# Kernel optimization log

Measured on AMD Instinct MI355X. Metric: run time of the kernel, lower is better.

## Reference

```python
import jax, jax.numpy as jnp
import numpy as np

B, S, H = 8, 512, 1024
NH = 8
DH = H // NH            # 128
INTER = 3072            # DebertaConfig default intermediate_size
SPAN = 512              # max_relative_positions (= max_position_embeddings)
LSTM_H = H // 2         # 512
EPS = 1e-7              # DeBERTa layer_norm_eps


def _ln(x, g, b):
    m = jnp.mean(x, -1, keepdims=True)
    v = jnp.var(x, -1, keepdims=True)
    return (x - m) / jnp.sqrt(v + EPS) * g + b


def _lstm_dir(x, Wih, Whh, bih, bhh, reverse):
    # x: [B,S,D]; precompute input projection for all steps
    xW = jnp.einsum('bsd,gd->sbg', x, Wih) + bih + bhh      # [S,B,4*Hd]
    Hd = Whh.shape[1]

    def step(carry, gx):
        h, c = carry
        gates = gx + h @ Whh.T
        i, f, g, o = jnp.split(gates, 4, axis=-1)           # torch gate order i,f,g,o
        i = jax.nn.sigmoid(i); f = jax.nn.sigmoid(f); o = jax.nn.sigmoid(o)
        g = jnp.tanh(g)
        c = f * c + i * g
        h = o * jnp.tanh(c)
        return (h, c), h

    h0 = jnp.zeros((x.shape[0], Hd), x.dtype)
    _, hs = jax.lax.scan(step, (h0, h0), xW, reverse=reverse)
    return jnp.swapaxes(hs, 0, 1)                            # [B,S,Hd]


def setup_inputs() -> dict:
    key = jax.random.key(0)
    ks = iter(jax.random.split(key, 40))

    def rn(shape, s=0.02):
        return jax.random.normal(next(ks), shape, jnp.float32) * s

    return {
        'x': jax.random.normal(next(ks), (B, S, H), jnp.float32),
        'pos_emb': rn((SPAN, H)),
        'emb_ln_g': jnp.ones((H,), jnp.float32),
        'emb_ln_b': jnp.zeros((H,), jnp.float32),
        'in_proj_w': rn((3 * H, H)),
        'q_bias': jnp.zeros((H,), jnp.float32),
        'v_bias': jnp.zeros((H,), jnp.float32),
        'rel_emb': rn((2 * SPAN, H)),
        'pos_proj_w': rn((H, H)),
        'pos_q_proj_w': rn((H, H)),
        'pos_q_proj_b': jnp.zeros((H,), jnp.float32),
        'attn_out_w': rn((H, H)),
        'attn_out_b': jnp.zeros((H,), jnp.float32),
        'attn_ln_g': jnp.ones((H,), jnp.float32),
        'attn_ln_b': jnp.zeros((H,), jnp.float32),
        'inter_w': rn((INTER, H)),
        'inter_b': jnp.zeros((INTER,), jnp.float32),
        'ffn_out_w': rn((H, INTER)),
        'ffn_out_b': jnp.zeros((H,), jnp.float32),
        'ffn_ln_g': jnp.ones((H,), jnp.float32),
        'ffn_ln_b': jnp.zeros((H,), jnp.float32),
        'Wih_f': rn((4 * LSTM_H, H)),
        'Whh_f': rn((4 * LSTM_H, LSTM_H)),
        'bih_f': jnp.zeros((4 * LSTM_H,), jnp.float32),
        'bhh_f': jnp.zeros((4 * LSTM_H,), jnp.float32),
        'Wih_r': rn((4 * LSTM_H, H)),
        'Whh_r': rn((4 * LSTM_H, LSTM_H)),
        'bih_r': jnp.zeros((4 * LSTM_H,), jnp.float32),
        'bhh_r': jnp.zeros((4 * LSTM_H,), jnp.float32),
    }


def reference(x, pos_emb, emb_ln_g, emb_ln_b, in_proj_w, q_bias, v_bias, rel_emb,
              pos_proj_w, pos_q_proj_w, pos_q_proj_b, attn_out_w, attn_out_b,
              attn_ln_g, attn_ln_b, inter_w, inter_b, ffn_out_w, ffn_out_b,
              ffn_ln_g, ffn_ln_b, Wih_f, Whh_f, bih_f, bhh_f, Wih_r, Whh_r,
              bih_r, bhh_r):
    # ---- DeBERTa embeddings: inputs_embeds + absolute positions, LayerNorm ----
    h = _ln(x + pos_emb[None, :S], emb_ln_g, emb_ln_b)

    # ---- disentangled self-attention (c2p + p2c) ----
    qkv = h @ in_proj_w.T                                    # [B,S,3H]
    q, k, v = jnp.split(qkv, 3, -1)
    q = q + q_bias
    v = v + v_bias

    def heads(t):
        return t.reshape(B, S, NH, DH).transpose(0, 2, 1, 3)  # [B,NH,S,DH]
    q, k, v = heads(q), heads(k), heads(v)

    scale_factor = 3.0                                       # 1 + len(['c2p','p2c'])
    q = q / jnp.sqrt(jnp.float32(DH) * scale_factor)
    scores = jnp.einsum('bhqd,bhkd->bhqk', q, k)             # [B,NH,S,S]

    rel_pos = jnp.arange(S)[:, None] - jnp.arange(S)[None, :]  # [S,S]

    # content -> position
    c2p_idx = jnp.clip(rel_pos + SPAN, 0, 2 * SPAN - 1)
    pos_key = (rel_emb @ pos_proj_w.T).reshape(2 * SPAN, NH, DH)
    c2p = jnp.einsum('bhqd,rhd->bhqr', q, pos_key)           # [B,NH,S,2*SPAN]
    c2p = jnp.take_along_axis(c2p, jnp.broadcast_to(c2p_idx[None, None], (B, NH, S, S)), axis=-1)

    # position -> content
    pos_q = (rel_emb @ pos_q_proj_w.T + pos_q_proj_b).reshape(2 * SPAN, NH, DH)
    pos_q = pos_q / jnp.sqrt(jnp.float32(DH) * scale_factor)
    p2c_idx = jnp.clip(-rel_pos + SPAN, 0, 2 * SPAN - 1)
    p2c = jnp.einsum('bhkd,rhd->bhkr', k, pos_q)             # [B,NH,S,2*SPAN]
    p2c = jnp.take_along_axis(p2c, jnp.broadcast_to(p2c_idx[None, None], (B, NH, S, S)), axis=-1)
    p2c = jnp.swapaxes(p2c, -1, -2)

    probs = jax.nn.softmax(scores + c2p + p2c, -1)
    ctx = jnp.einsum('bhqk,bhkd->bhqd', probs, v).transpose(0, 2, 1, 3).reshape(B, S, H)

    h = _ln(ctx @ attn_out_w.T + attn_out_b + h, attn_ln_g, attn_ln_b)
    inter = jax.nn.gelu(h @ inter_w.T + inter_b, approximate=False)
    h = _ln(inter @ ffn_out_w.T + ffn_out_b + h, ffn_ln_g, ffn_ln_b)

    # ---- bidirectional single-layer LSTM ----
    hf = _lstm_dir(h, Wih_f, Whh_f, bih_f, bhh_f, False)
    hr = _lstm_dir(h, Wih_r, Whh_r, bih_r, bhh_r, True)
    return jnp.concatenate([hf, hr], -1)                     # [B,S,H]
```

## Files before the change

kernel.cpp:

```cpp
#include <hip/hip_runtime.h>
#include <cstdint>


typedef __bf16 bf8_t __attribute__((ext_vector_type(8)));
typedef float f32x4 __attribute__((ext_vector_type(4)));
typedef unsigned int u32x4 __attribute__((ext_vector_type(4)));

__device__ __forceinline__ unsigned short f2bf(float f) {
  union { float f; unsigned int u; } v; v.f = f;
  unsigned int r = v.u + 0x7fffu + ((v.u >> 16) & 1u);
  return (unsigned short)(r >> 16);
}
__device__ __forceinline__ float bf2f(unsigned short s) {
  union { unsigned int u; float f; } v; v.u = ((unsigned int)s) << 16;
  return v.f;
}
__device__ __forceinline__ float bflo(unsigned int u) {
  union { unsigned int u; float f; } v; v.u = u << 16; return v.f;
}
__device__ __forceinline__ float bfhi(unsigned int u) {
  union { unsigned int u; float f; } v; v.u = u & 0xffff0000u; return v.f;
}

__device__ __forceinline__ void async16(const void* g, void* l) {
  __builtin_amdgcn_global_load_lds(
      (const __attribute__((address_space(1))) void*)g,
      (__attribute__((address_space(3))) void*)l, 16, 0, 0);
}

__device__ __forceinline__ void ld2_ic(const unsigned short* p0,
                                       const unsigned short* p1,
                                       u32x4& r0, u32x4& r1) {
  asm volatile("global_load_dwordx4 %0, %2, off sc0 sc1\n\t"
               "global_load_dwordx4 %1, %3, off sc0 sc1\n\t"
               "s_waitcnt vmcnt(0)"
               : "=v"(r0), "=v"(r1)
               : "v"(p0), "v"(p1)
               : "memory");
}
__device__ __forceinline__ void st_ic(unsigned short* p, u32x4 v) {
  asm volatile("global_store_dwordx4 %0, %1, off sc0 sc1"
               :: "v"(p), "v"(v) : "memory");
}
__device__ __forceinline__ int ld_flag_ic(const int* p) {
  int r;
  asm volatile("global_load_dword %0, %1, off sc0 sc1\n\t"
               "s_waitcnt vmcnt(0)"
               : "=v"(r) : "v"(p) : "memory");
  return r;
}
__device__ __forceinline__ void wait_vm0() {
  asm volatile("s_waitcnt vmcnt(0)" ::: "memory");
}

__global__ void k_sentinel(float* out) { out[0] = 1e30f; }

__global__ void k_cast_bf16(const float* __restrict__ in, unsigned short* __restrict__ out) {
  long i = ((long)blockIdx.x * 256 + threadIdx.x) * 4;
  float4 v = *(const float4*)(in + i);
  unsigned int a = (unsigned int)f2bf(v.x) | ((unsigned int)f2bf(v.y) << 16);
  unsigned int b = (unsigned int)f2bf(v.z) | ((unsigned int)f2bf(v.w) << 16);
  *(uint2*)(out + i) = make_uint2(a, b);
}

__global__ void k_build_bias(const float* qb, const float* vb, float* qkvBias,
                             const float* bihf, const float* bhhf, float* bsf,
                             const float* bihr, const float* bhhr, float* bsr) {
  int i = blockIdx.x * 256 + threadIdx.x;
  if (i < 3072) {
    float v;
    if (i < 1024) v = qb[i];
    else if (i < 2048) v = 0.f;
    else v = vb[i - 2048];
    qkvBias[i] = v;
  }
  if (i < 2048) {
    bsf[i] = bihf[i] + bhhf[i];
    bsr[i] = bihr[i] + bhhr[i];
  }
}

__global__ __launch_bounds__(256) void k_layernorm(
    const float* __restrict__ in, const float* __restrict__ res, unsigned int resMask,
    const float* __restrict__ gamma, const float* __restrict__ beta,
    float* __restrict__ outF, unsigned short* __restrict__ outB) {
  const int row = blockIdx.x;
  const int tid = threadIdx.x;
  float4 v = ((const float4*)(in + (long)row * 1024))[tid];
  if (res) {
    float4 r = ((const float4*)(res + (long)(row & resMask) * 1024))[tid];
    v.x += r.x; v.y += r.y; v.z += r.z; v.w += r.w;
  }
  float s = v.x + v.y + v.z + v.w;
  float q = v.x * v.x + v.y * v.y + v.z * v.z + v.w * v.w;
#pragma unroll
  for (int o = 32; o; o >>= 1) { s += __shfl_down(s, o); q += __shfl_down(q, o); }
  __shared__ float rs[4], rq[4];
  const int wave = tid >> 6, lane = tid & 63;
  if (lane == 0) { rs[wave] = s; rq[wave] = q; }
  __syncthreads();
  s = rs[0] + rs[1] + rs[2] + rs[3];
  q = rq[0] + rq[1] + rq[2] + rq[3];
  const float mean = s * (1.f / 1024.f);
  const float var = q * (1.f / 1024.f) - mean * mean;
  const float rstd = rsqrtf(var + 1e-7f);
  float4 g4 = ((const float4*)gamma)[tid];
  float4 b4 = ((const float4*)beta)[tid];
  float4 o4;
  o4.x = (v.x - mean) * rstd * g4.x + b4.x;
  o4.y = (v.y - mean) * rstd * g4.y + b4.y;
  o4.z = (v.z - mean) * rstd * g4.z + b4.z;
  o4.w = (v.w - mean) * rstd * g4.w + b4.w;
  if (outF) ((float4*)(outF + (long)row * 1024))[tid] = o4;
  if (outB) {
    unsigned int a = (unsigned int)f2bf(o4.x) | ((unsigned int)f2bf(o4.y) << 16);
    unsigned int b = (unsigned int)f2bf(o4.z) | ((unsigned int)f2bf(o4.w) << 16);
    ((uint2*)(outB + (long)row * 1024))[tid] = make_uint2(a, b);
  }
}

template <int MODE>
__global__ __launch_bounds__(256) void k_gemm_bt(
    const unsigned short* __restrict__ A, int lda,
    const unsigned short* __restrict__ Bm, int ldb,
    void* __restrict__ Cv, int ldc,
    int K, const float* __restrict__ bias, float scale) {
  __shared__ __align__(16) unsigned short As[128 * 32];
  __shared__ __align__(16) unsigned short Bs[128 * 32];
  const int tid = threadIdx.x;
  const int lane = tid & 63;
  const int wave = tid >> 6;
  const int n0 = blockIdx.x * 128;
  const int m0 = blockIdx.y * 128;
  const int srow = tid >> 2;
  const int scol = (tid & 3) * 8;
  const unsigned short* ag0 = A + (long)(m0 + srow) * lda + scol;
  const unsigned short* ag1 = A + (long)(m0 + 64 + srow) * lda + scol;
  const unsigned short* bg0 = Bm + (long)(n0 + srow) * ldb + scol;
  const unsigned short* bg1 = Bm + (long)(n0 + 64 + srow) * ldb + scol;
  unsigned short* asd0 = &As[(wave * 16) * 32];
  unsigned short* asd1 = &As[(64 + wave * 16) * 32];
  unsigned short* bsd0 = &Bs[(wave * 16) * 32];
  unsigned short* bsd1 = &Bs[(64 + wave * 16) * 32];
  const int wm = wave >> 1, wn = wave & 1;
  const int mrow = lane & 15;
  const int kq = (lane >> 4) * 8;
  const f32x4 vzero = {0.f, 0.f, 0.f, 0.f};
  f32x4 acc[4][4];
#pragma unroll
  for (int i = 0; i < 4; ++i)
#pragma unroll
    for (int j = 0; j < 4; ++j) acc[i][j] = vzero;

  const int nk = K >> 5;
  for (int kt = 0; kt < nk; ++kt) {
    if (kt) __syncthreads();
    async16(ag0, asd0); async16(ag1, asd1);
    async16(bg0, bsd0); async16(bg1, bsd1);
    ag0 += 32; ag1 += 32; bg0 += 32; bg1 += 32;
    __syncthreads();
    bf8_t af[4], bf[4];
#pragma unroll
    for (int i = 0; i < 4; ++i)
      af[i] = *(const bf8_t*)&As[(wm * 64 + i * 16 + mrow) * 32 + kq];
#pragma unroll
    for (int j = 0; j < 4; ++j)
      bf[j] = *(const bf8_t*)&Bs[(wn * 64 + j * 16 + mrow) * 32 + kq];
#pragma unroll
    for (int i = 0; i < 4; ++i)
#pragma unroll
      for (int j = 0; j < 4; ++j)
        acc[i][j] = __builtin_amdgcn_mfma_f32_16x16x32_bf16(af[i], bf[j], acc[i][j], 0, 0, 0);
  }
  const int quad = lane >> 4;
  const int cn = lane & 15;
  float* Cf = (float*)Cv;
  unsigned short* Cb = (unsigned short*)Cv;
#pragma unroll
  for (int i = 0; i < 4; ++i) {
#pragma unroll
    for (int j = 0; j < 4; ++j) {
#pragma unroll
      for (int r = 0; r < 4; ++r) {
        int row = m0 + wm * 64 + i * 16 + quad * 4 + r;
        int col = n0 + wn * 64 + j * 16 + cn;
        float v = acc[i][j][r];
        if (bias) v += bias[col];
        v *= scale;
        if (MODE == 2) v = 0.5f * v * (1.0f + erff(v * 0.70710678118654752f));
        long idx = (long)row * ldc + col;
        if (MODE == 0) Cf[idx] = v;
        else Cb[idx] = f2bf(v);
      }
    }
  }
}

__global__ __launch_bounds__(256) void k_attention(
    const unsigned short* __restrict__ qkv,
    const unsigned short* __restrict__ c2p,
    const unsigned short* __restrict__ p2c,
    unsigned short* __restrict__ ctx, int h) {
  const int tid = threadIdx.x;
  const int qt = blockIdx.x;
  const int b = blockIdx.y;
  const int q0 = qt * 16;
  __shared__ __align__(16) float sc[16][520];
  __shared__ __align__(16) float qs[16][128];

  for (int i = tid; i < 16 * 128; i += 256) {
    int ql = i >> 7, d = i & 127;
    qs[ql][d] = bf2f(qkv[((long)(b * 512 + q0 + ql)) * 3072 + h * 128 + d]);
  }
  __syncthreads();

  const float scale = 0.051031036307982884f;
  for (int pass = 0; pass < 2; ++pass) {
    const int k = tid + pass * 256;
    float4 kvf[32];
    const unsigned short* kp = qkv + ((long)(b * 512 + k)) * 3072 + 1024 + h * 128;
#pragma unroll
    for (int c = 0; c < 16; ++c) {
      uint4 u = ((const uint4*)kp)[c];
      kvf[2 * c + 0] = make_float4(bflo(u.x), bfhi(u.x), bflo(u.y), bfhi(u.y));
      kvf[2 * c + 1] = make_float4(bflo(u.z), bfhi(u.z), bflo(u.w), bfhi(u.w));
    }
    const unsigned short* pp = p2c + ((long)(b * 512 + k)) * 1024 + (q0 - k + 512);
    for (int ql = 0; ql < 16; ++ql) {
      float dot = 0.f;
#pragma unroll
      for (int dd = 0; dd < 32; ++dd) {
        float4 qf = ((const float4*)&qs[ql][0])[dd];
        dot += qf.x * kvf[dd].x + qf.y * kvf[dd].y + qf.z * kvf[dd].z + qf.w * kvf[dd].w;
      }
      sc[ql][k] = dot * scale + bf2f(pp[ql]);
    }
  }
  __syncthreads();

  const int wave = tid >> 6, lane = tid & 63;
#pragma unroll
  for (int rr = 0; rr < 4; ++rr) {
    const int r = wave * 4 + rr;
    const int q = q0 + r;
    const unsigned short* cp = c2p + ((long)(b * 512 + q)) * 1024 + (q + 512);
    float v[8];
#pragma unroll
    for (int i = 0; i < 8; ++i) {
      int k = lane + 64 * i;
      v[i] = sc[r][k] + bf2f(cp[-k]);
    }
    float m = v[0];
#pragma unroll
    for (int i = 1; i < 8; ++i) m = fmaxf(m, v[i]);
#pragma unroll
    for (int o = 32; o; o >>= 1) m = fmaxf(m, __shfl_xor(m, o));
    float ssum = 0.f;
#pragma unroll
    for (int i = 0; i < 8; ++i) { v[i] = __expf(v[i] - m); ssum += v[i]; }
#pragma unroll
    for (int o = 32; o; o >>= 1) ssum += __shfl_xor(ssum, o);
    const float inv = 1.0f / ssum;
#pragma unroll
    for (int i = 0; i < 8; ++i) sc[r][lane + 64 * i] = v[i] * inv;
  }
  __syncthreads();

  const int d = tid & 127;
  const int qg = tid >> 7;
  float acc[8] = {0, 0, 0, 0, 0, 0, 0, 0};
  const unsigned short* vp = qkv + ((long)(b * 512)) * 3072 + 2048 + h * 128 + d;
  for (int k = 0; k < 512; k += 4) {
    float v0 = bf2f(vp[(long)(k + 0) * 3072]);
    float v1 = bf2f(vp[(long)(k + 1) * 3072]);
    float v2 = bf2f(vp[(long)(k + 2) * 3072]);
    float v3 = bf2f(vp[(long)(k + 3) * 3072]);
#pragma unroll
    for (int qq = 0; qq < 8; ++qq) {
      float4 p = *(const float4*)&sc[qg * 8 + qq][k];
      acc[qq] += p.x * v0 + p.y * v1 + p.z * v2 + p.w * v3;
    }
  }
#pragma unroll
  for (int qq = 0; qq < 8; ++qq) {
    int q = q0 + qg * 8 + qq;
    ctx[((long)(b * 512 + q)) * 1024 + h * 128 + d] = f2bf(acc[qq]);
  }
}

__global__ __launch_bounds__(256) void k_lstm(
    const float* __restrict__ WhhF, const float* __restrict__ WhhR,
    const unsigned short* __restrict__ xWF, const unsigned short* __restrict__ xWR,
    float* __restrict__ out, unsigned short* __restrict__ hx,
    int* __restrict__ flags) {
  const int tid = threadIdx.x;
  const int lane = tid & 63;
  const int g = tid >> 6;
  const int dir = blockIdx.y;
  const int j0 = blockIdx.x * 16;
  const float* Whh = dir ? WhhR : WhhF;
  const unsigned short* xW = dir ? xWR : xWF;
  int* flg = flags + dir * 512;
  unsigned short* hxd = hx + (long)dir * 512 * 8 * 512;

  __shared__ __align__(16) unsigned short hT[16][520];
  __shared__ float gl[4][16][8];
  __shared__ __align__(16) unsigned short hs[8][16];

  const int m = lane & 15, quad = lane >> 4;
  bf8_t afr[16];
  {
    const float* wr = Whh + ((long)(g * 512 + j0 + m)) * 512 + quad * 8;
#pragma unroll
    for (int kt = 0; kt < 16; ++kt) {
      float4 f0 = *(const float4*)(wr + kt * 32);
      float4 f1 = *(const float4*)(wr + kt * 32 + 4);
      bf8_t a;
      a[0] = (__bf16)f0.x; a[1] = (__bf16)f0.y; a[2] = (__bf16)f0.z; a[3] = (__bf16)f0.w;
      a[4] = (__bf16)f1.x; a[5] = (__bf16)f1.y; a[6] = (__bf16)f1.z; a[7] = (__bf16)f1.w;
      afr[kt] = a;
    }
  }
  for (int i = tid; i < 16 * 520; i += 256) (&hT[0][0])[i] = 0;
  float cstate = 0.f;
  __syncthreads();

  for (int se = 0; se < 512; ++se) {
    const int s = dir ? 511 - se : se;
    uint2 uxw = make_uint2(0u, 0u);
    if (m < 8)
      uxw = *(const uint2*)(xW + ((long)(m * 512 + s)) * 2048 + g * 512 + j0 + quad * 4);

    if (se) {
      const int sp = dir ? s + 1 : s - 1;
      if (tid == 0) {
        while (ld_flag_ic(flg + (se - 1)) < 32) __builtin_amdgcn_s_sleep(1);
      }
      __syncthreads();
      const unsigned short* hxs = hxd + (long)sp * 4096;
      const int bb = tid >> 6;
      const int jc = (tid & 63) * 8;
      u32x4 r0, r1;
      ld2_ic(hxs + bb * 512 + jc, hxs + (bb + 4) * 512 + jc, r0, r1);
      *(u32x4*)&hT[bb][jc] = r0;
      *(u32x4*)&hT[bb + 4][jc] = r1;
      __syncthreads();
    }

    f32x4 acc0 = {0.f, 0.f, 0.f, 0.f}, acc1 = {0.f, 0.f, 0.f, 0.f};
#pragma unroll
    for (int t = 0; t < 8; ++t) {
      bf8_t b0 = *(const bf8_t*)&hT[m][(2 * t) * 32 + quad * 8];
      bf8_t b1 = *(const bf8_t*)&hT[m][(2 * t + 1) * 32 + quad * 8];
      acc0 = __builtin_amdgcn_mfma_f32_16x16x32_bf16(afr[2 * t], b0, acc0, 0, 0, 0);
      acc1 = __builtin_amdgcn_mfma_f32_16x16x32_bf16(afr[2 * t + 1], b1, acc1, 0, 0, 0);
    }
    if (m < 8) {
      gl[g][quad * 4 + 0][m] = acc0[0] + acc1[0] + bflo(uxw.x);
      gl[g][quad * 4 + 1][m] = acc0[1] + acc1[1] + bfhi(uxw.x);
      gl[g][quad * 4 + 2][m] = acc0[2] + acc1[2] + bflo(uxw.y);
      gl[g][quad * 4 + 3][m] = acc0[3] + acc1[3] + bfhi(uxw.y);
    }
    __syncthreads();
    if (tid < 128) {
      const int jj = tid >> 3, bb = tid & 7;
      float iv = gl[0][jj][bb], fv = gl[1][jj][bb];
      float gv = gl[2][jj][bb], ov = gl[3][jj][bb];
      float is = 1.f / (1.f + __expf(-iv));
      float fs = 1.f / (1.f + __expf(-fv));
      float gt = tanhf(gv);
      float os = 1.f / (1.f + __expf(-ov));
      cstate = fs * cstate + is * gt;
      float hv = os * tanhf(cstate);
      out[((long)(bb * 512 + s)) * 1024 + dir * 512 + j0 + jj] = hv;
      hs[bb][jj] = f2bf(hv);
    }
    __syncthreads();
    if (tid < 16) {
      const int b = tid >> 1, half = tid & 1;
      st_ic(hxd + (long)s * 4096 + b * 512 + j0 + half * 8,
            *(const u32x4*)&hs[b][half * 8]);
    }
    wait_vm0();
    __syncthreads();
    if (tid == 0)
      __hip_atomic_fetch_add(flg + se, 1, __ATOMIC_RELAXED, __HIP_MEMORY_SCOPE_AGENT);
  }
}

extern "C" void kernel_launch(void* const* d_in, const int* in_sizes, int n_in,
                              void* d_out, int out_size, void* d_ws, size_t ws_size,
                              hipStream_t stream) {
  const float* x         = (const float*)d_in[0];
  const float* pos_emb   = (const float*)d_in[1];
  const float* emb_ln_g  = (const float*)d_in[2];
  const float* emb_ln_b  = (const float*)d_in[3];
  const float* in_proj_w = (const float*)d_in[4];
  const float* q_bias    = (const float*)d_in[5];
  const float* v_bias    = (const float*)d_in[6];
  const float* rel_emb   = (const float*)d_in[7];
  const float* pos_proj_w   = (const float*)d_in[8];
  const float* pos_q_proj_w = (const float*)d_in[9];
  const float* pos_q_proj_b = (const float*)d_in[10];
  const float* attn_out_w = (const float*)d_in[11];
  const float* attn_out_b = (const float*)d_in[12];
  const float* attn_ln_g  = (const float*)d_in[13];
  const float* attn_ln_b  = (const float*)d_in[14];
  const float* inter_w    = (const float*)d_in[15];
  const float* inter_b    = (const float*)d_in[16];
  const float* ffn_out_w  = (const float*)d_in[17];
  const float* ffn_out_b  = (const float*)d_in[18];
  const float* ffn_ln_g   = (const float*)d_in[19];
  const float* ffn_ln_b   = (const float*)d_in[20];
  const float* Wih_f = (const float*)d_in[21];
  const float* Whh_f = (const float*)d_in[22];
  const float* bih_f = (const float*)d_in[23];
  const float* bhh_f = (const float*)d_in[24];
  const float* Wih_r = (const float*)d_in[25];
  const float* Whh_r = (const float*)d_in[26];
  const float* bih_r = (const float*)d_in[27];
  const float* bhh_r = (const float*)d_in[28];
  float* out = (float*)d_out;

  const size_t MB = 1ull << 20;
  const size_t NEED = 85 * MB;
  if (ws_size < NEED) {
    k_sentinel<<<dim3(1), dim3(1), 0, stream>>>(out);
    return;
  }
  char* ws = (char*)d_ws;
  typedef unsigned short u16;
  u16*   qkv_b    = (u16*)(ws + 0);
  float* attn_tmp = (float*)(ws + 0);
  u16*   xW_f     = (u16*)(ws + 0);
  u16*   h1_b     = (u16*)(ws + 16 * MB);
  u16*   xW_r     = (u16*)(ws + 16 * MB);
  float* h0_f     = (float*)(ws + 24 * MB);
  u16*   inter_bf = (u16*)(ws + 24 * MB);
  u16*   hx       = (u16*)(ws + 32 * MB);
  u16*   c2p_h    = (u16*)(ws + 40 * MB);
  u16*   p2c_h    = (u16*)(ws + 48 * MB);
  float* h1_f     = (float*)(ws + 48 * MB);
  u16*   h0_b     = (u16*)(ws + 64 * MB);
  u16*   ctx_b    = (u16*)(ws + 64 * MB);
  u16*   h2_b     = (u16*)(ws + 64 * MB);
  u16*   wscr     = (u16*)(ws + 72 * MB);
  u16*   relemb_b = (u16*)(ws + 78 * MB);
  u16*   poskey_b = (u16*)(ws + 80 * MB);
  u16*   posq_b   = (u16*)(ws + 82 * MB);
  float* bias_qkv = (float*)(ws + 84 * MB);
  float* bsum_f   = (float*)(ws + 84 * MB + 16 * 1024);
  float* bsum_r   = (float*)(ws + 84 * MB + 32 * 1024);
  int*   flags    = (int*)(ws + 84 * MB + 48 * 1024);
  float* ffn_tmp  = out;

  const float SCALE = 0.051031036307982884f;

  hipMemsetAsync(flags, 0, 1024 * 4, stream);

  auto cast = [&](const float* src, u16* dst, long n) {
    k_cast_bf16<<<dim3((unsigned)(n / 1024)), dim3(256), 0, stream>>>(src, dst);
  };

  k_build_bias<<<dim3(12), dim3(256), 0, stream>>>(q_bias, v_bias, bias_qkv,
                                                   bih_f, bhh_f, bsum_f,
                                                   bih_r, bhh_r, bsum_r);

  k_layernorm<<<dim3(4096), dim3(256), 0, stream>>>(x, pos_emb, 511u, emb_ln_g,
                                                    emb_ln_b, h0_f, h0_b);

  cast(in_proj_w, wscr, 3145728L);
  k_gemm_bt<1><<<dim3(24, 32), dim3(256), 0, stream>>>(
      h0_b, 1024, wscr, 1024, qkv_b, 3072, 1024, bias_qkv, 1.0f);

  cast(rel_emb, relemb_b, 1048576L);
  cast(pos_proj_w, wscr, 1048576L);
  k_gemm_bt<1><<<dim3(8, 8), dim3(256), 0, stream>>>(
      relemb_b, 1024, wscr, 1024, poskey_b, 1024, 1024, (const float*)nullptr, 1.0f);
  cast(pos_q_proj_w, wscr, 1048576L);
  k_gemm_bt<1><<<dim3(8, 8), dim3(256), 0, stream>>>(
      relemb_b, 1024, wscr, 1024, posq_b, 1024, 1024, pos_q_proj_b, SCALE);

  for (int h = 0; h < 8; ++h) {
    k_gemm_bt<1><<<dim3(8, 32), dim3(256), 0, stream>>>(
        qkv_b + h * 128, 3072, poskey_b + h * 128, 1024, c2p_h, 1024, 128,
        (const float*)nullptr, SCALE);
    k_gemm_bt<1><<<dim3(8, 32), dim3(256), 0, stream>>>(
        qkv_b + 1024 + h * 128, 3072, posq_b + h * 128, 1024, p2c_h, 1024, 128,
        (const float*)nullptr, 1.0f);
    k_attention<<<dim3(32, 8), dim3(256), 0, stream>>>(qkv_b, c2p_h, p2c_h, ctx_b, h);
  }

  cast(attn_out_w, wscr, 1048576L);
  k_gemm_bt<0><<<dim3(8, 32), dim3(256), 0, stream>>>(
      ctx_b, 1024, wscr, 1024, attn_tmp, 1024, 1024, attn_out_b, 1.0f);
  k_layernorm<<<dim3(4096), dim3(256), 0, stream>>>(attn_tmp, h0_f, 0xFFFFFFFFu,
                                                    attn_ln_g, attn_ln_b, h1_f, h1_b);

  cast(inter_w, wscr, 3145728L);
  k_gemm_bt<2><<<dim3(24, 32), dim3(256), 0, stream>>>(
      h1_b, 1024, wscr, 1024, inter_bf, 3072, 1024, inter_b, 1.0f);
  cast(ffn_out_w, wscr, 3145728L);
  k_gemm_bt<0><<<dim3(8, 32), dim3(256), 0, stream>>>(
      inter_bf, 3072, wscr, 3072, ffn_tmp, 1024, 3072, ffn_out_b, 1.0f);
  k_layernorm<<<dim3(4096), dim3(256), 0, stream>>>(ffn_tmp, h1_f, 0xFFFFFFFFu,
                                                    ffn_ln_g, ffn_ln_b,
                                                    (float*)nullptr, h2_b);

  cast(Wih_f, wscr, 2097152L);
  k_gemm_bt<1><<<dim3(16, 32), dim3(256), 0, stream>>>(
      h2_b, 1024, wscr, 1024, xW_f, 2048, 1024, bsum_f, 1.0f);
  cast(Wih_r, wscr, 2097152L);
  k_gemm_bt<1><<<dim3(16, 32), dim3(256), 0, stream>>>(
      h2_b, 1024, wscr, 1024, xW_r, 2048, 1024, bsum_r, 1.0f);

  k_lstm<<<dim3(32, 2), dim3(256), 0, stream>>>(Whh_f, Whh_r, xW_f, xW_r, out, hx, flags);

  (void)in_sizes; (void)n_in; (void)out_size;
}
```

Baseline: 2.440 ms.

## Replace LSTM flag counter sync with data-embedded nonzero sentinel polling

Removes the per-step atomic flag counter and its store-wait-barrier-atomic chain in the persistent LSTM kernel. Consumers now poll the hidden-state buffer directly, which is zeroed beforehand, until every bf16 value is nonzero, relying on forcing the low mantissa bit of each stored h to 1. The change also splits the MFMA accumulation into four independent chains and replaces tanhf with an exp-based formula. It adds a memset of the 8MB hx buffer and perturbs h by one bf16 ulp, and it assumes the 16-byte stores become visible atomically.

```diff
diff --git a/kernel.cpp b/kernel.cpp
--- a/kernel.cpp
+++ b/kernel.cpp
@@ -41,16 +41,6 @@
 __device__ __forceinline__ void st_ic(unsigned short* p, u32x4 v) {
   asm volatile("global_store_dwordx4 %0, %1, off sc0 sc1"
                :: "v"(p), "v"(v) : "memory");
-}
-__device__ __forceinline__ int ld_flag_ic(const int* p) {
-  int r;
-  asm volatile("global_load_dword %0, %1, off sc0 sc1\n\t"
-               "s_waitcnt vmcnt(0)"
-               : "=v"(r) : "v"(p) : "memory");
-  return r;
-}
-__device__ __forceinline__ void wait_vm0() {
-  asm volatile("s_waitcnt vmcnt(0)" ::: "memory");
 }
 
 __global__ void k_sentinel(float* out) { out[0] = 1e30f; }
@@ -291,8 +281,7 @@
 __global__ __launch_bounds__(256) void k_lstm(
     const float* __restrict__ WhhF, const float* __restrict__ WhhR,
     const unsigned short* __restrict__ xWF, const unsigned short* __restrict__ xWR,
-    float* __restrict__ out, unsigned short* __restrict__ hx,
-    int* __restrict__ flags) {
+    float* __restrict__ out, unsigned short* __restrict__ hx) {
   const int tid = threadIdx.x;
   const int lane = tid & 63;
   const int g = tid >> 6;
@@ -300,8 +289,7 @@
   const int j0 = blockIdx.x * 16;
   const float* Whh = dir ? WhhR : WhhF;
   const unsigned short* xW = dir ? xWR : xWF;
-  int* flg = flags + dir * 512;
-  unsigned short* hxd = hx + (long)dir * 512 * 8 * 512;
+  unsigned short* hxd = hx + (long)dir * 512 * 4096;
 
   __shared__ __align__(16) unsigned short hT[16][520];
   __shared__ float gl[4][16][8];
@@ -333,33 +321,42 @@
 
     if (se) {
       const int sp = dir ? s + 1 : s - 1;
-      if (tid == 0) {
-        while (ld_flag_ic(flg + (se - 1)) < 32) __builtin_amdgcn_s_sleep(1);
+      const unsigned short* hxs = hxd + (long)sp * 4096;
+      const unsigned short* p0 = hxs + (2 * g) * 512 + lane * 8;
+      const unsigned short* p1 = hxs + (2 * g + 1) * 512 + lane * 8;
+      u32x4 r0, r1;
+      for (;;) {
+        ld2_ic(p0, p1, r0, r1);
+        bool ok = true;
+#pragma unroll
+        for (int t = 0; t < 4; ++t) {
+          ok = ok && (r0[t] & 0xffffu) && (r0[t] >> 16) &&
+               (r1[t] & 0xffffu) && (r1[t] >> 16);
+        }
+        if (__ballot(ok) == 0xFFFFFFFFFFFFFFFFull) break;
       }
+      *(u32x4*)&hT[2 * g][lane * 8] = r0;
+      *(u32x4*)&hT[2 * g + 1][lane * 8] = r1;
       __syncthreads();
-      const unsigned short* hxs = hxd + (long)sp * 4096;
-      const int bb = tid >> 6;
-      const int jc = (tid & 63) * 8;
-      u32x4 r0, r1;
-      ld2_ic(hxs + bb * 512 + jc, hxs + (bb + 4) * 512 + jc, r0, r1);
-      *(u32x4*)&hT[bb][jc] = r0;
-      *(u32x4*)&hT[bb + 4][jc] = r1;
-      __syncthreads();
-    }
-
-    f32x4 acc0 = {0.f, 0.f, 0.f, 0.f}, acc1 = {0.f, 0.f, 0.f, 0.f};
-#pragma unroll
-    for (int t = 0; t < 8; ++t) {
-      bf8_t b0 = *(const bf8_t*)&hT[m][(2 * t) * 32 + quad * 8];
-      bf8_t b1 = *(const bf8_t*)&hT[m][(2 * t + 1) * 32 + quad * 8];
-      acc0 = __builtin_amdgcn_mfma_f32_16x16x32_bf16(afr[2 * t], b0, acc0, 0, 0, 0);
-      acc1 = __builtin_amdgcn_mfma_f32_16x16x32_bf16(afr[2 * t + 1], b1, acc1, 0, 0, 0);
+    }
+
+    f32x4 a0 = {0.f, 0.f, 0.f, 0.f}, a1 = a0, a2 = a0, a3 = a0;
+#pragma unroll
+    for (int t = 0; t < 4; ++t) {
+      bf8_t b0 = *(const bf8_t*)&hT[m][(4 * t + 0) * 32 + quad * 8];
+      bf8_t b1 = *(const bf8_t*)&hT[m][(4 * t + 1) * 32 + quad * 8];
+      bf8_t b2 = *(const bf8_t*)&hT[m][(4 * t + 2) * 32 + quad * 8];
+      bf8_t b3 = *(const bf8_t*)&hT[m][(4 * t + 3) * 32 + quad * 8];
+      a0 = __builtin_amdgcn_mfma_f32_16x16x32_bf16(afr[4 * t + 0], b0, a0, 0, 0, 0);
+      a1 = __builtin_amdgcn_mfma_f32_16x16x32_bf16(afr[4 * t + 1], b1, a1, 0, 0, 0);
+      a2 = __builtin_amdgcn_mfma_f32_16x16x32_bf16(afr[4 * t + 2], b2, a2, 0, 0, 0);
+      a3 = __builtin_amdgcn_mfma_f32_16x16x32_bf16(afr[4 * t + 3], b3, a3, 0, 0, 0);
     }
     if (m < 8) {
-      gl[g][quad * 4 + 0][m] = acc0[0] + acc1[0] + bflo(uxw.x);
-      gl[g][quad * 4 + 1][m] = acc0[1] + acc1[1] + bfhi(uxw.x);
-      gl[g][quad * 4 + 2][m] = acc0[2] + acc1[2] + bflo(uxw.y);
-      gl[g][quad * 4 + 3][m] = acc0[3] + acc1[3] + bfhi(uxw.y);
+      gl[g][quad * 4 + 0][m] = a0[0] + a1[0] + a2[0] + a3[0] + bflo(uxw.x);
+      gl[g][quad * 4 + 1][m] = a0[1] + a1[1] + a2[1] + a3[1] + bfhi(uxw.x);
+      gl[g][quad * 4 + 2][m] = a0[2] + a1[2] + a2[2] + a3[2] + bflo(uxw.y);
+      gl[g][quad * 4 + 3][m] = a0[3] + a1[3] + a2[3] + a3[3] + bfhi(uxw.y);
     }
     __syncthreads();
     if (tid < 128) {
@@ -368,12 +365,12 @@
       float gv = gl[2][jj][bb], ov = gl[3][jj][bb];
       float is = 1.f / (1.f + __expf(-iv));
       float fs = 1.f / (1.f + __expf(-fv));
-      float gt = tanhf(gv);
+      float gt = 2.f / (1.f + __expf(-2.f * gv)) - 1.f;
       float os = 1.f / (1.f + __expf(-ov));
       cstate = fs * cstate + is * gt;
-      float hv = os * tanhf(cstate);
+      float hv = os * (2.f / (1.f + __expf(-2.f * cstate)) - 1.f);
+      hs[bb][jj] = f2bf(hv) | 1;
       out[((long)(bb * 512 + s)) * 1024 + dir * 512 + j0 + jj] = hv;
-      hs[bb][jj] = f2bf(hv);
     }
     __syncthreads();
     if (tid < 16) {
@@ -381,10 +378,6 @@
       st_ic(hxd + (long)s * 4096 + b * 512 + j0 + half * 8,
             *(const u32x4*)&hs[b][half * 8]);
     }
-    wait_vm0();
-    __syncthreads();
-    if (tid == 0)
-      __hip_atomic_fetch_add(flg + se, 1, __ATOMIC_RELAXED, __HIP_MEMORY_SCOPE_AGENT);
   }
 }
 
@@ -451,12 +444,9 @@
   float* bias_qkv = (float*)(ws + 84 * MB);
   float* bsum_f   = (float*)(ws + 84 * MB + 16 * 1024);
   float* bsum_r   = (float*)(ws + 84 * MB + 32 * 1024);
-  int*   flags    = (int*)(ws + 84 * MB + 48 * 1024);
   float* ffn_tmp  = out;
 
   const float SCALE = 0.051031036307982884f;
-
-  hipMemsetAsync(flags, 0, 1024 * 4, stream);
 
   auto cast = [&](const float* src, u16* dst, long n) {
     k_cast_bf16<<<dim3((unsigned)(n / 1024)), dim3(256), 0, stream>>>(src, dst);
@@ -503,6 +493,7 @@
   cast(ffn_out_w, wscr, 3145728L);
   k_gemm_bt<0><<<dim3(8, 32), dim3(256), 0, stream>>>(
       inter_bf, 3072, wscr, 3072, ffn_tmp, 1024, 3072, ffn_out_b, 1.0f);
+  hipMemsetAsync(hx, 0, 8 * MB, stream);
   k_layernorm<<<dim3(4096), dim3(256), 0, stream>>>(ffn_tmp, h1_f, 0xFFFFFFFFu,
                                                     ffn_ln_g, ffn_ln_b,
                                                     (float*)nullptr, h2_b);
@@ -514,7 +505,7 @@
   k_gemm_bt<1><<<dim3(16, 32), dim3(256), 0, stream>>>(
       h2_b, 1024, wscr, 1024, xW_r, 2048, 1024, bsum_r, 1.0f);
 
-  k_lstm<<<dim3(32, 2), dim3(256), 0, stream>>>(Whh_f, Whh_r, xW_f, xW_r, out, hx, flags);
+  k_lstm<<<dim3(32, 2), dim3(256), 0, stream>>>(Whh_f, Whh_r, xW_f, xW_r, out, hx);
 
   (void)in_sizes; (void)n_in; (void)out_size;
 }
```

Result: faster. 2.312 ms (-5.2%).
